# Performance work log

Hardware: AMD Instinct MI355X
Metric: run time of the kernel (lower is better)

## Reference

```python
import jax, jax.numpy as jnp
import numpy as np

LN_EPS = 1e-5
NORM_EPS = 1e-12  # F.normalize eps


def _l2norm(x):
    # torch F.normalize(p=2, dim=-1): x / max(||x||, eps)
    n = jnp.sqrt(jnp.sum(x * x, axis=-1, keepdims=True))
    return x / jnp.maximum(n, NORM_EPS)


def setup_inputs() -> dict:
    key = jax.random.key(0)
    D, R, H = 256, 32, 64  # d_model, rank, d_model//4
    B, C, P = 32, 64, 96
    ks = jax.random.split(key, 16)
    s = 0.05
    return {
        "x": jax.random.normal(ks[0], (B * C, P, D), jnp.float32),
        "ln_gamma": jnp.ones((D,), jnp.float32),
        "ln_beta": jnp.zeros((D,), jnp.float32),
        "Wd": jax.random.normal(ks[1], (D, R), jnp.float32) * s,
        "bd": jax.random.normal(ks[2], (R,), jnp.float32) * s,
        "Wq": jax.random.normal(ks[3], (R, R), jnp.float32) * s,
        "Wk": jax.random.normal(ks[4], (R, R), jnp.float32) * s,
        "Wv": jax.random.normal(ks[5], (R, R), jnp.float32) * s,
        "Wg": jax.random.normal(ks[6], (R, R), jnp.float32) * s,
        "bg": jax.random.normal(ks[7], (R,), jnp.float32) * s,
        "Wu": jax.random.normal(ks[8], (R, D), jnp.float32) * s,
        "bu": jax.random.normal(ks[9], (D,), jnp.float32) * s,
        "W1": jax.random.normal(ks[10], (D, H), jnp.float32) * s,
        "b1": jax.random.normal(ks[11], (H,), jnp.float32) * s,
        "W2": jax.random.normal(ks[12], (H, D), jnp.float32) * s,
        "b2": jnp.full((D,), -5.0, jnp.float32),  # gate_init bias
        "B": B,
        "C": C,
    }


def reference(x, ln_gamma, ln_beta, Wd, bd, Wq, Wk, Wv, Wg, bg, Wu, bu, W1, b1, W2, b2, B, C):
    BC, P, D = x.shape
    # [B*C, P, D] -> [B*P, C, D] channel-mixing layout
    h = x.reshape(B, C, P, D).transpose(0, 2, 1, 3).reshape(B * P, C, D)

    # LayerNorm over D (biased variance, as in torch LayerNorm)
    mu = jnp.mean(h, axis=-1, keepdims=True)
    var = jnp.var(h, axis=-1, keepdims=True)
    h_norm = (h - mu) * jax.lax.rsqrt(var + LN_EPS) * ln_gamma + ln_beta

    # bottleneck projection to rank R
    h_low = h_norm @ Wd + bd  # [BP, C, R]

    # Hydra linear attention: cosine-normalized Q/K, sum-pooled K*V global feature
    Q = _l2norm(h_low @ Wq)
    K = _l2norm(h_low @ Wk)
    V = h_low @ Wv
    global_feat = jnp.sum(K * V, axis=1, keepdims=True)  # [BP, 1, R]
    h_attn = Q * global_feat

    # content gate and up-projection
    gate_c = jax.nn.sigmoid(h_low @ Wg + bg)
    mixed = (h_attn * gate_c) @ Wu + bu  # [BP, C, D]

    # AdaptiveGate: unbiased variance over channel dim (torch .var default ddof=1)
    chan_var = jnp.var(h, axis=1, ddof=1)  # [BP, D]
    gate_logits = jax.nn.gelu(chan_var @ W1 + b1, approximate=False) @ W2 + b2
    gate = jax.nn.sigmoid(gate_logits)[:, None, :]  # [BP, 1, D]

    out = h + gate * mixed
    # back to [B*C, P, D]
    return out.reshape(B, P, C, D).transpose(0, 2, 1, 3).reshape(BC, P, D)
```

## Files before the change

### kernel.cpp

```cpp
#include <hip/hip_runtime.h>
#include <hip/hip_bf16.h>

#define DD 256
#define RR 32
#define CC 64
#define PB 96
#define NT 1024

typedef __attribute__((ext_vector_type(8))) short short8;
typedef __attribute__((ext_vector_type(4))) float f32x4;

__device__ __forceinline__ short f2bf(float f) {
    return __builtin_bit_cast(short, __float2bfloat16(f));
}
__device__ __forceinline__ float b2f(unsigned short s) {
    union { unsigned u; float f; } v; v.u = ((unsigned)s) << 16;
    return v.f;
}

__device__ __forceinline__ int hswz(int c, int d) {
    return c * 256 + (d ^ ((c & 7) << 3));
}
__device__ __forceinline__ int nswz(int r, int k) {
    return r * 32 + (k ^ (((r >> 1) & 3) << 3));
}

__global__ __launch_bounds__(1024, 1)
void prep_kernel(const float* __restrict__ ln_g, const float* __restrict__ ln_b,
                 const float* __restrict__ Wd, const float* __restrict__ bd,
                 const float* __restrict__ Wq, const float* __restrict__ Wk,
                 const float* __restrict__ Wv, const float* __restrict__ Wg,
                 const float* __restrict__ Wu,
                 const float* __restrict__ W1, const float* __restrict__ W2,
                 short* __restrict__ wsWd, short* __restrict__ wsQKVG,
                 short* __restrict__ wsWu, float* __restrict__ wsLN,
                 float* __restrict__ wsW1T, float* __restrict__ wsW2T)
{
    __shared__ float redp[2048];
    const int t = threadIdx.x;
    {
        const int r = t >> 5, dblk = t & 31;
        short8 vv;
        float sa = 0.f, sb = 0.f;
        #pragma unroll
        for (int j = 0; j < 8; ++j) {
            const int d = dblk * 8 + j;
            const float wd = Wd[d * RR + r];
            const float g  = ln_g[d];
            vv[j] = f2bf(g * wd);
            sa += g * wd;
            sb += ln_b[d] * wd;
        }
        *(short8*)&wsWd[r * 256 + ((dblk ^ (r & 7)) << 3)] = vv;
        redp[r * 32 + dblk]        = sa;
        redp[1024 + r * 32 + dblk] = sb;
    }
    if (t < 512) {
        const int m = t >> 7, rr2 = (t >> 2) & 31, kg = t & 3;
        const float* Wm = (m == 0) ? Wq : (m == 1) ? Wk : (m == 2) ? Wv : Wg;
        short8 vv;
        #pragma unroll
        for (int j = 0; j < 8; ++j)
            vv[j] = f2bf(Wm[(kg * 8 + j) * RR + rr2]);
        *(short8*)&wsQKVG[m * 1024 + rr2 * 32 + ((kg ^ ((rr2 >> 1) & 3)) << 3)] = vv;
    }
    {
        const int d = t & 255, kg = t >> 8;
        short8 vv;
        #pragma unroll
        for (int j = 0; j < 8; ++j)
            vv[j] = f2bf(Wu[(kg * 8 + j) * DD + d]);
        *(short8*)&wsWu[d * 32 + ((kg ^ ((d >> 1) & 3)) << 3)] = vv;
    }
    #pragma unroll
    for (int rep = 0; rep < 16; ++rep) {
        const int id = rep * 1024 + t;
        const int j = id >> 8, d = id & 255;
        wsW1T[j * 256 + d] = W1[d * 64 + j];
    }
    #pragma unroll
    for (int rep = 0; rep < 16; ++rep) {
        const int id = rep * 1024 + t;
        const int d = id >> 6, j = id & 63;
        wsW2T[d * 64 + j] = W2[j * 256 + d];
    }
    __syncthreads();
    if (t < 32) {
        float s = 0.f;
        #pragma unroll
        for (int g = 0; g < 32; ++g) s += redp[t * 32 + g];
        wsLN[t] = s;
    } else if (t < 64) {
        const int r = t - 32;
        float s = 0.f;
        #pragma unroll
        for (int g = 0; g < 32; ++g) s += redp[1024 + r * 32 + g];
        wsLN[t] = s + bd[r];
    }
}

__global__ __launch_bounds__(NT, 8)
void hydra_kernel(const float* __restrict__ x,
                  const short* __restrict__ wsWd, const short* __restrict__ wsQKVG,
                  const short* __restrict__ wsWu, const float* __restrict__ wsLN,
                  const float* __restrict__ wsW1T, const float* __restrict__ wsW2T,
                  const float* __restrict__ bg,
                  const float* __restrict__ bu,
                  const float* __restrict__ b1, const float* __restrict__ b2,
                  float* __restrict__ out)
{
    __shared__ short hbf[CC * DD];
    __shared__ short wreg[RR * DD];
    __shared__ short qg[CC * RR];
    __shared__ short lowbuf[CC * RR];
    __shared__ float redA[1024];
    __shared__ float redB[2048];
    __shared__ float redC[1024];
    __shared__ float mu_s[CC], rstd_s[CC];
    __shared__ float cv_s[DD], gate_s[DD];
    __shared__ float hid_s[64];
    __shared__ float ln_a[RR], ln_bv[RR];

    const int t    = threadIdx.x;
    const int lane = t & 63;
    const int w    = t >> 6;
    const int bp   = blockIdx.x;
    const int b    = bp / PB;
    const int p    = bp - b * PB;
    const size_t rowbase = (size_t)(b * CC) * PB * DD + (size_t)p * DD;

    #pragma unroll
    for (int i = 0; i < 4; ++i) {
        const int c = w * 4 + i;
        const float4 v = *(const float4*)(x + rowbase + (size_t)c * (PB * DD) + 4 * lane);
        float s1 = v.x + v.y + v.z + v.w;
        float s2 = v.x * v.x + v.y * v.y + v.z * v.z + v.w * v.w;
        s1 += __shfl_xor(s1, 1, 64); s2 += __shfl_xor(s2, 1, 64);
        s1 += __shfl_xor(s1, 2, 64); s2 += __shfl_xor(s2, 2, 64);
        s1 += __shfl_xor(s1, 4, 64); s2 += __shfl_xor(s2, 4, 64);
        if ((lane & 7) == 0)
            *(float2*)&redC[(c * 8 + (lane >> 3)) * 2] = make_float2(s1, s2);
        ushort4 pk;
        pk.x = (unsigned short)f2bf(v.x); pk.y = (unsigned short)f2bf(v.y);
        pk.z = (unsigned short)f2bf(v.z); pk.w = (unsigned short)f2bf(v.w);
        *(ushort4*)&hbf[hswz(c, 4 * lane)] = pk;
    }
    *(short8*)&wreg[t * 8] = *(const short8*)&wsWd[t * 8];
    if (t < 32)              ln_a[t]       = wsLN[t];
    else if (t < 64)         ln_bv[t - 32] = wsLN[t];
    __syncthreads();

    f32x4 s3acc = {0.f, 0.f, 0.f, 0.f};
    if (w < 8) {
        const int ct = w >> 1, rt = w & 1;
        const int arow = ct * 16 + (lane & 15);
        const int brow = rt * 16 + (lane & 15);
        const int ksub = lane >> 4;
        #pragma unroll
        for (int step = 0; step < 8; ++step) {
            const short8 a  = *(const short8*)&hbf[hswz(arow, step * 32 + ksub * 8)];
            const short8 bf = *(const short8*)&wreg[hswz(brow, step * 32 + ksub * 8)];
            s3acc = __builtin_amdgcn_mfma_f32_16x16x32_bf16(a, bf, s3acc, 0, 0, 0);
        }
    } else {
        const int idx = t - 512;
        const int dp  = idx & 127;
        const int rg  = idx >> 7;
        const int d0  = dp * 2;
        float s1a = 0.f, s1b = 0.f, s2a = 0.f, s2b = 0.f;
        #pragma unroll
        for (int i = 0; i < 16; ++i) {
            const int c = rg * 16 + i;
            const ushort2 u = *(const ushort2*)&hbf[hswz(c, d0)];
            const float va = b2f(u.x), vb = b2f(u.y);
            s1a += va; s2a += va * va;
            s1b += vb; s2b += vb * vb;
        }
        *(float2*)&redB[rg * 256 + d0]        = make_float2(s1a, s1b);
        *(float2*)&redB[1024 + rg * 256 + d0] = make_float2(s2a, s2b);
        if (idx < 64) {
            const int c = idx;
            float s1 = 0.f, s2 = 0.f;
            #pragma unroll
            for (int g = 0; g < 8; ++g) {
                const float2 pr = *(const float2*)&redC[(c * 8 + g) * 2];
                s1 += pr.x; s2 += pr.y;
            }
            const float mu = s1 * (1.f / 256.f);
            mu_s[c]   = mu;
            rstd_s[c] = rsqrtf(s2 * (1.f / 256.f) - mu * mu + 1e-5f);
        }
    }
    __syncthreads();

    if (w < 8) {
        const int ct = w >> 1, rt = w & 1;
        const int col = rt * 16 + (lane & 15);
        const float la = ln_a[col], lb = ln_bv[col];
        #pragma unroll
        for (int i = 0; i < 4; ++i) {
            const int c = ct * 16 + (lane >> 4) * 4 + i;
            const float rs = rstd_s[c];
            const float hl = rs * s3acc[i] - rs * mu_s[c] * la + lb;
            lowbuf[nswz(c, col)] = f2bf(hl);
        }
    } else {
        const int idx = t - 512;
        *(short8*)&wreg[idx * 8] = *(const short8*)&wsQKVG[idx * 8];
    }
    if (t < 256) {
        const float S1 = redB[t] + redB[256 + t] + redB[512 + t] + redB[768 + t];
        const float S2 = redB[1024 + t] + redB[1280 + t] + redB[1536 + t] + redB[1792 + t];
        cv_s[t] = (S2 - S1 * S1 * (1.f / 64.f)) * (1.f / 63.f);
    }
    __syncthreads();

    if (w < 8) {
        const int ct = w >> 1, pair = w & 1;
        const int mA = pair ? 1 : 0;
        const int mB = pair ? 2 : 3;
        const int arow = ct * 16 + (lane & 15);
        const int ksub = lane >> 4;
        const short8 a = *(const short8*)&lowbuf[nswz(arow, ksub * 8)];
        f32x4 aA0 = {0,0,0,0}, aA1 = {0,0,0,0}, aB0 = {0,0,0,0}, aB1 = {0,0,0,0};
        {
            const int br0 = (lane & 15), br1 = 16 + (lane & 15);
            const short8 bA0 = *(const short8*)&wreg[mA * 1024 + nswz(br0, ksub * 8)];
            const short8 bA1 = *(const short8*)&wreg[mA * 1024 + nswz(br1, ksub * 8)];
            const short8 bB0 = *(const short8*)&wreg[mB * 1024 + nswz(br0, ksub * 8)];
            const short8 bB1 = *(const short8*)&wreg[mB * 1024 + nswz(br1, ksub * 8)];
            aA0 = __builtin_amdgcn_mfma_f32_16x16x32_bf16(a, bA0, aA0, 0, 0, 0);
            aA1 = __builtin_amdgcn_mfma_f32_16x16x32_bf16(a, bA1, aA1, 0, 0, 0);
            aB0 = __builtin_amdgcn_mfma_f32_16x16x32_bf16(a, bB0, aB0, 0, 0, 0);
            aB1 = __builtin_amdgcn_mfma_f32_16x16x32_bf16(a, bB1, aB1, 0, 0, 0);
        }
        float qs[4];
        #pragma unroll
        for (int i = 0; i < 4; ++i) {
            float ss = aA0[i] * aA0[i] + aA1[i] * aA1[i];
            ss += __shfl_xor(ss, 1, 64);
            ss += __shfl_xor(ss, 2, 64);
            ss += __shfl_xor(ss, 4, 64);
            ss += __shfl_xor(ss, 8, 64);
            qs[i] = 1.f / fmaxf(sqrtf(ss), 1e-12f);
        }
        const int col0 = (lane & 15), col1 = 16 + (lane & 15);
        if (pair == 0) {
            const float bgv0 = bg[col0], bgv1 = bg[col1];
            #pragma unroll
            for (int i = 0; i < 4; ++i) {
                const int c = ct * 16 + (lane >> 4) * 4 + i;
                const float g0 = 1.f / (1.f + __expf(-(aB0[i] + bgv0)));
                const float g1 = 1.f / (1.f + __expf(-(aB1[i] + bgv1)));
                qg[c * 32 + col0] = f2bf(aA0[i] * qs[i] * g0);
                qg[c * 32 + col1] = f2bf(aA1[i] * qs[i] * g1);
            }
        } else {
            #pragma unroll
            for (int i = 0; i < 4; ++i) {
                const int c = ct * 16 + (lane >> 4) * 4 + i;
                redB[c * 32 + col0] = aA0[i] * qs[i] * aB0[i];
                redB[c * 32 + col1] = aA1[i] * qs[i] * aB1[i];
            }
        }
    } else {
        const int idx = t - 512;
        const int j = idx & 63, dg = idx >> 6;
        const float* w1row = wsW1T + j * 256 + dg * 32;
        float s = 0.f;
        #pragma unroll
        for (int ii = 0; ii < 8; ++ii) {
            const float4 wv = *(const float4*)(w1row + ii * 4);
            const float4 cvv = *(const float4*)&cv_s[dg * 32 + ii * 4];
            s += cvv.x * wv.x + cvv.y * wv.y + cvv.z * wv.z + cvv.w * wv.w;
        }
        redA[dg * 64 + j] = s;
    }
    __syncthreads();

    if (t < 64) {
        float s = b1[t];
        #pragma unroll
        for (int g = 0; g < 8; ++g) s += redA[g * 64 + t];
        hid_s[t] = 0.5f * s * (1.f + erff(s * 0.70710678118654752f));
    }
    if (t >= 256 && t < 512) {
        const int idx = t - 256;
        const int r = idx & 31, g = idx >> 5;
        float s = 0.f;
        #pragma unroll
        for (int i = 0; i < 8; ++i)
            s += redB[(g * 8 + i) * 32 + r];
        redA[512 + g * 32 + r] = s;
    }
    *(short8*)&wreg[t * 8] = *(const short8*)&wsWu[t * 8];
    __syncthreads();

    if (t < 256) {
        const int r = t & 31, c0 = t >> 5, c1 = (t >> 5) + 32;
        float gf = 0.f;
        #pragma unroll
        for (int g = 0; g < 8; ++g) gf += redA[512 + g * 32 + r];
        lowbuf[nswz(c0, r)] = f2bf(b2f((unsigned short)qg[c0 * 32 + r]) * gf);
        lowbuf[nswz(c1, r)] = f2bf(b2f((unsigned short)qg[c1 * 32 + r]) * gf);
    } else if (t < 512) {
        const int d = t - 256;
        const float* w2row = wsW2T + d * 64;
        float s = b2[d];
        #pragma unroll
        for (int ii = 0; ii < 16; ++ii) {
            const float4 wv = *(const float4*)(w2row + ii * 4);
            const float4 hv = *(const float4*)&hid_s[ii * 4];
            s += hv.x * wv.x + hv.y * wv.y + hv.z * wv.z + hv.w * wv.w;
        }
        gate_s[d] = 1.f / (1.f + __expf(-s));
    }
    __syncthreads();

    {
        const int ct = w & 3, dg = w >> 2;
        const int arow = ct * 16 + (lane & 15);
        const int ksub = lane >> 4;
        const short8 a = *(const short8*)&lowbuf[nswz(arow, ksub * 8)];
        #pragma unroll
        for (int j = 0; j < 4; ++j) {
            const int col = (dg * 4 + j) * 16 + (lane & 15);
            const short8 bf = *(const short8*)&wreg[nswz(col, ksub * 8)];
            f32x4 acc = {0.f, 0.f, 0.f, 0.f};
            acc = __builtin_amdgcn_mfma_f32_16x16x32_bf16(a, bf, acc, 0, 0, 0);
            const float gt  = gate_s[col];
            const float buv = bu[col];
            #pragma unroll
            for (int i = 0; i < 4; ++i) {
                const int c = ct * 16 + (lane >> 4) * 4 + i;
                const float xv = b2f((unsigned short)hbf[hswz(c, col)]);
                out[rowbase + (size_t)c * (PB * DD) + col] = xv + gt * (acc[i] + buv);
            }
        }
    }
}

extern "C" void kernel_launch(void* const* d_in, const int* in_sizes, int n_in,
                              void* d_out, int out_size, void* d_ws, size_t ws_size,
                              hipStream_t stream) {
    (void)in_sizes; (void)n_in; (void)out_size; (void)ws_size;
    const float* x    = (const float*)d_in[0];
    const float* ln_g = (const float*)d_in[1];
    const float* ln_b = (const float*)d_in[2];
    const float* Wd   = (const float*)d_in[3];
    const float* bd   = (const float*)d_in[4];
    const float* Wq   = (const float*)d_in[5];
    const float* Wk   = (const float*)d_in[6];
    const float* Wv   = (const float*)d_in[7];
    const float* Wg   = (const float*)d_in[8];
    const float* bg   = (const float*)d_in[9];
    const float* Wu   = (const float*)d_in[10];
    const float* bu   = (const float*)d_in[11];
    const float* W1   = (const float*)d_in[12];
    const float* b1   = (const float*)d_in[13];
    const float* W2   = (const float*)d_in[14];
    const float* b2   = (const float*)d_in[15];
    float* out = (float*)d_out;

    short* wsWd   = (short*)d_ws;
    short* wsQKVG = wsWd + 8192;
    short* wsWu   = wsQKVG + 4096;
    float* wsLN   = (float*)(wsWd + 20480);
    float* wsW1T  = wsLN + 64;
    float* wsW2T  = wsW1T + 16384;

    prep_kernel<<<dim3(1), dim3(1024), 0, stream>>>(
        ln_g, ln_b, Wd, bd, Wq, Wk, Wv, Wg, Wu, W1, W2,
        wsWd, wsQKVG, wsWu, wsLN, wsW1T, wsW2T);
    hydra_kernel<<<dim3(32 * PB), dim3(NT), 0, stream>>>(
        x, wsWd, wsQKVG, wsWu, wsLN, wsW1T, wsW2T, bg, bu, b1, b2, out);
}
```

Before: 163.1 us.

## Replace shared-memory reductions with wave shuffles and read Wu fragments from global

The global K*V feature and the W1 hidden-layer dot products are now reduced with cross-lane shuffles instead of being written to shared memory and summed in a separate phase. This removes one block-wide barrier and a shared-memory round trip. Wu is pre-laid-out in the prep kernel in MFMA fragment order, so the final matmul loads its B operand straight from global or cache instead of first staging it into LDS. This trades LDS traffic for per-wave global loads that should mostly hit in cache.

```diff
diff --git a/kernel.cpp b/kernel.cpp
--- a/kernel.cpp
+++ b/kernel.cpp
@@ -33,7 +33,7 @@
                  const float* __restrict__ Wu,
                  const float* __restrict__ W1, const float* __restrict__ W2,
                  short* __restrict__ wsWd, short* __restrict__ wsQKVG,
-                 short* __restrict__ wsWu, float* __restrict__ wsLN,
+                 short* __restrict__ wsF3, float* __restrict__ wsLN,
                  float* __restrict__ wsW1T, float* __restrict__ wsW2T)
 {
     __shared__ float redp[2048];
@@ -65,12 +65,15 @@
         *(short8*)&wsQKVG[m * 1024 + rr2 * 32 + ((kg ^ ((rr2 >> 1) & 3)) << 3)] = vv;
     }
     {
-        const int d = t & 255, kg = t >> 8;
-        short8 vv;
-        #pragma unroll
-        for (int j = 0; j < 8; ++j)
-            vv[j] = f2bf(Wu[(kg * 8 + j) * DD + d]);
-        *(short8*)&wsWu[d * 32 + ((kg ^ ((d >> 1) & 3)) << 3)] = vv;
+        const int f = t >> 6, l = t & 63;
+        const int d = f * 16 + (l & 15);
+        short8 v;
+        #pragma unroll
+        for (int j = 0; j < 8; ++j) {
+            const int r = (l >> 4) * 8 + j;
+            v[j] = f2bf(Wu[r * DD + d]);
+        }
+        *(short8*)&wsF3[f * 512 + l * 8] = v;
     }
     #pragma unroll
     for (int rep = 0; rep < 16; ++rep) {
@@ -102,7 +105,7 @@
 __global__ __launch_bounds__(NT, 8)
 void hydra_kernel(const float* __restrict__ x,
                   const short* __restrict__ wsWd, const short* __restrict__ wsQKVG,
-                  const short* __restrict__ wsWu, const float* __restrict__ wsLN,
+                  const short* __restrict__ wsF3, const float* __restrict__ wsLN,
                   const float* __restrict__ wsW1T, const float* __restrict__ wsW2T,
                   const float* __restrict__ bg,
                   const float* __restrict__ bu,
@@ -113,9 +116,9 @@
     __shared__ short wreg[RR * DD];
     __shared__ short qg[CC * RR];
     __shared__ short lowbuf[CC * RR];
-    __shared__ float redA[1024];
     __shared__ float redB[2048];
     __shared__ float redC[1024];
+    __shared__ float gfp[128];
     __shared__ float mu_s[CC], rstd_s[CC];
     __shared__ float cv_s[DD], gate_s[DD];
     __shared__ float hid_s[64];
@@ -256,51 +259,43 @@
                 qg[c * 32 + col1] = f2bf(aA1[i] * qs[i] * g1);
             }
         } else {
+            float p0 = 0.f, p1 = 0.f;
             #pragma unroll
             for (int i = 0; i < 4; ++i) {
-                const int c = ct * 16 + (lane >> 4) * 4 + i;
-                redB[c * 32 + col0] = aA0[i] * qs[i] * aB0[i];
-                redB[c * 32 + col1] = aA1[i] * qs[i] * aB1[i];
+                p0 += (aA0[i] * qs[i]) * aB0[i];
+                p1 += (aA1[i] * qs[i]) * aB1[i];
+            }
+            p0 += __shfl_xor(p0, 16, 64); p1 += __shfl_xor(p1, 16, 64);
+            p0 += __shfl_xor(p0, 32, 64); p1 += __shfl_xor(p1, 32, 64);
+            if (lane < 16) {
+                gfp[ct * 32 + lane]      = p0;
+                gfp[ct * 32 + 16 + lane] = p1;
             }
         }
     } else {
-        const int idx = t - 512;
-        const int j = idx & 63, dg = idx >> 6;
-        const float* w1row = wsW1T + j * 256 + dg * 32;
+        const int j = (w - 8) * 8 + (lane >> 3);
+        const int q = lane & 7;
+        const float* w1row = wsW1T + j * 256 + q * 32;
         float s = 0.f;
         #pragma unroll
         for (int ii = 0; ii < 8; ++ii) {
-            const float4 wv = *(const float4*)(w1row + ii * 4);
-            const float4 cvv = *(const float4*)&cv_s[dg * 32 + ii * 4];
+            const float4 wv  = *(const float4*)(w1row + ii * 4);
+            const float4 cvv = *(const float4*)&cv_s[q * 32 + ii * 4];
             s += cvv.x * wv.x + cvv.y * wv.y + cvv.z * wv.z + cvv.w * wv.w;
         }
-        redA[dg * 64 + j] = s;
-    }
-    __syncthreads();
-
-    if (t < 64) {
-        float s = b1[t];
-        #pragma unroll
-        for (int g = 0; g < 8; ++g) s += redA[g * 64 + t];
-        hid_s[t] = 0.5f * s * (1.f + erff(s * 0.70710678118654752f));
-    }
-    if (t >= 256 && t < 512) {
-        const int idx = t - 256;
-        const int r = idx & 31, g = idx >> 5;
-        float s = 0.f;
-        #pragma unroll
-        for (int i = 0; i < 8; ++i)
-            s += redB[(g * 8 + i) * 32 + r];
-        redA[512 + g * 32 + r] = s;
-    }
-    *(short8*)&wreg[t * 8] = *(const short8*)&wsWu[t * 8];
+        s += __shfl_xor(s, 1, 64);
+        s += __shfl_xor(s, 2, 64);
+        s += __shfl_xor(s, 4, 64);
+        if (q == 0) {
+            const float z = s + b1[j];
+            hid_s[j] = 0.5f * z * (1.f + erff(z * 0.70710678118654752f));
+        }
+    }
     __syncthreads();
 
     if (t < 256) {
         const int r = t & 31, c0 = t >> 5, c1 = (t >> 5) + 32;
-        float gf = 0.f;
-        #pragma unroll
-        for (int g = 0; g < 8; ++g) gf += redA[512 + g * 32 + r];
+        const float gf = gfp[r] + gfp[32 + r] + gfp[64 + r] + gfp[96 + r];
         lowbuf[nswz(c0, r)] = f2bf(b2f((unsigned short)qg[c0 * 32 + r]) * gf);
         lowbuf[nswz(c1, r)] = f2bf(b2f((unsigned short)qg[c1 * 32 + r]) * gf);
     } else if (t < 512) {
@@ -324,8 +319,9 @@
         const short8 a = *(const short8*)&lowbuf[nswz(arow, ksub * 8)];
         #pragma unroll
         for (int j = 0; j < 4; ++j) {
-            const int col = (dg * 4 + j) * 16 + (lane & 15);
-            const short8 bf = *(const short8*)&wreg[nswz(col, ksub * 8)];
+            const int dt = dg * 4 + j;
+            const int col = dt * 16 + (lane & 15);
+            const short8 bf = *(const short8*)(wsF3 + dt * 512 + lane * 8);
             f32x4 acc = {0.f, 0.f, 0.f, 0.f};
             acc = __builtin_amdgcn_mfma_f32_16x16x32_bf16(a, bf, acc, 0, 0, 0);
             const float gt  = gate_s[col];
@@ -364,14 +360,14 @@
 
     short* wsWd   = (short*)d_ws;
     short* wsQKVG = wsWd + 8192;
-    short* wsWu   = wsQKVG + 4096;
+    short* wsF3   = wsQKVG + 4096;
     float* wsLN   = (float*)(wsWd + 20480);
     float* wsW1T  = wsLN + 64;
     float* wsW2T  = wsW1T + 16384;
 
     prep_kernel<<<dim3(1), dim3(1024), 0, stream>>>(
         ln_g, ln_b, Wd, bd, Wq, Wk, Wv, Wg, Wu, W1, W2,
-        wsWd, wsQKVG, wsWu, wsLN, wsW1T, wsW2T);
+        wsWd, wsQKVG, wsF3, wsLN, wsW1T, wsW2T);
     hydra_kernel<<<dim3(32 * PB), dim3(NT), 0, stream>>>(
-        x, wsWd, wsQKVG, wsWu, wsLN, wsW1T, wsW2T, bg, bu, b1, b2, out);
-}
+        x, wsWd, wsQKVG, wsF3, wsLN, wsW1T, wsW2T, bg, bu, b1, b2, out);
+}
```

Result: faster. 159.6 us (-2.2%).
